# Performance work log

Hardware: AMD Instinct MI355X
Metric: run time of the kernel (lower is better)

Reference implementation:

```python
import itertools
import jax, jax.numpy as jnp
import numpy as np

N_QUBITS = 8
N_LAYERS = 2
BATCH = 8192
INPUT_DIM = 3072
NUM_CLASSES = 10

_In = np.eye(2, dtype=np.complex64)
_Xn = np.array([[0, 1], [1, 0]], dtype=np.complex64)
_Yn = np.array([[0, -1j], [1j, 0]], dtype=np.complex64)
_Zn = np.array([[1, 0], [0, -1]], dtype=np.complex64)
_P = {"I": _In, "X": _Xn, "Y": _Yn, "Z": _Zn}
_XX = jnp.asarray(np.kron(_Xn, _Xn))
_YY = jnp.asarray(np.kron(_Yn, _Yn))
_ZZ = jnp.asarray(np.kron(_Zn, _Zn))
_I4 = jnp.eye(4, dtype=jnp.complex64)
# 2-qubit Pauli words in PennyLane ArbitraryUnitary order: IX, IY, IZ, XI, ..., ZZ
_WORDS = jnp.asarray(np.stack([np.kron(_P[a], _P[b]) for a, b in itertools.product("IXYZ", repeat=2)][1:]))


def apply_gate(state, U, wires):
    """Apply a 2^k x 2^k gate U to the given wires of a (2,)*n statevector."""
    n = state.ndim
    k = len(wires)
    U = U.reshape((2,) * (2 * k)).astype(state.dtype)
    state = jnp.tensordot(U, state, axes=(list(range(k, 2 * k)), list(wires)))
    rest = [a for a in range(n) if a not in wires]
    perm = [0] * n
    for i, a in enumerate(wires):
        perm[a] = i
    for j, a in enumerate(rest):
        perm[a] = k + j
    return jnp.transpose(state, perm)


def u3_mat(t, p, d):
    ct, st = jnp.cos(t / 2).astype(jnp.complex64), jnp.sin(t / 2).astype(jnp.complex64)
    r0 = jnp.stack([ct, -jnp.exp(1j * d) * st])
    r1 = jnp.stack([jnp.exp(1j * p) * st, jnp.exp(1j * (p + d)) * ct])
    return jnp.stack([r0, r1])


def ry_mat(t):
    c, s = jnp.cos(t / 2), jnp.sin(t / 2)
    return jnp.stack([jnp.stack([c, -s]), jnp.stack([s, c])]).astype(jnp.complex64)


def ising_mat(phi, pauli2):
    # exp(-i phi/2 P) for two-qubit Pauli word P (P^2 = I)
    return jnp.cos(phi / 2) * _I4 - 1j * jnp.sin(phi / 2) * pauli2


def circuit(conv_w, pool_w, last_w, feats):
    state = jnp.zeros((2,) * N_QUBITS, jnp.complex64).at[(0,) * N_QUBITS].set(1.0)
    # AngleEmbedding with RY rotations
    for w in range(N_QUBITS):
        state = apply_gate(state, ry_mat(feats[w]), (w,))
    wires = list(range(N_QUBITS))
    for layer in range(N_LAYERS):
        cw = conv_w[layer]
        nw = len(wires)
        for p in (0, 1):
            for idx in range(nw - 1):
                if idx % 2 == p:
                    a, b = wires[idx], wires[idx + 1]
                    state = apply_gate(state, u3_mat(cw[idx, 0], cw[idx, 1], cw[idx, 2]), (a,))
                    state = apply_gate(state, u3_mat(cw[idx + 1, 3], cw[idx + 1, 4], cw[idx + 1, 5]), (b,))
                    state = apply_gate(state, ising_mat(cw[idx, 6], _ZZ), (a, b))
                    state = apply_gate(state, ising_mat(cw[idx, 7], _YY), (a, b))
                    state = apply_gate(state, ising_mat(cw[idx, 8], _XX), (a, b))
                    state = apply_gate(state, u3_mat(cw[idx, 9], cw[idx, 10], cw[idx, 11]), (a,))
                    state = apply_gate(state, u3_mat(cw[idx + 1, 12], cw[idx + 1, 13], cw[idx + 1, 14]), (b,))
        # Pooling: mid-circuit measure + conditional U3 == (deferred measurement)
        pw = pool_w[layer]
        for idx in range(1, nw, 2):
            u = u3_mat(pw[idx // 2, 0], pw[idx // 2, 1], pw[idx // 2, 2])
            cu = jnp.zeros((4, 4), jnp.complex64).at[0, 0].set(1.0).at[1, 1].set(1.0).at[2:, 2:].set(u)
            state = apply_gate(state, cu, (wires[idx], wires[idx - 1]))
        wires = wires[::2]
    # ArbitraryUnitary on remaining 2 wires: product of 15 PauliRot gates
    for k in range(15):
        mat = jnp.cos(last_w[k] / 2) * _I4 - 1j * jnp.sin(last_w[k] / 2) * _WORDS[k]
        state = apply_gate(state, mat, tuple(wires))
    probs = state.real ** 2 + state.imag ** 2
    z = jnp.sum(probs, axis=tuple(range(1, N_QUBITS)))  # (2,)
    return z[0] - z[1]


def setup_inputs() -> dict:
    key = jax.random.key(0)
    ks = jax.random.split(key, 8)
    return {
        "x": jax.random.normal(ks[0], (BATCH, INPUT_DIM), jnp.float32),
        "fc_w": jax.random.normal(ks[1], (N_QUBITS, INPUT_DIM), jnp.float32) * 0.02,
        "fc_b": jnp.zeros((N_QUBITS,), jnp.float32),
        "conv_params": jax.random.normal(ks[2], (N_LAYERS, N_QUBITS, 15), jnp.float32),
        "pool_params": jax.random.normal(ks[3], (N_LAYERS, N_QUBITS // 2, 3), jnp.float32),
        "last_params": jax.random.normal(ks[4], (15,), jnp.float32),
        "out_w": jax.random.normal(ks[5], (NUM_CLASSES, 1), jnp.float32),
        "out_b": jnp.zeros((NUM_CLASSES,), jnp.float32),
    }


def reference(x, fc_w, fc_b, conv_params, pool_params, last_params, out_w, out_b):
    feats = jnp.tanh(x.reshape(x.shape[0], -1) @ fc_w.T + fc_b)  # (B, n_qubits)
    qvals = jax.vmap(lambda f: circuit(conv_params, pool_params, last_params, f))(feats)
    logits = qvals[:, None].astype(x.dtype) @ out_w.T + out_b  # (B, num_classes)
    return logits
```

## Files before the change

kernel.cpp:

```cpp
#include <hip/hip_runtime.h>
#include <math.h>

__constant__ int G_ORD[17] = {0,1,2,3,4,5,6, 10,11,12,13, 7,8,9, 14,15, 16};
__constant__ int G_WA[17]  = {0,2,4,6,1,3,5, 1,3,5,7, 0,4,2, 2,6, 0};
__constant__ int G_WB[17]  = {1,3,5,7,2,4,6, 0,2,4,6, 2,6,4, 0,4, 4};
__constant__ int CDESC[10][3] = {{0,0,1},{0,2,3},{0,4,5},{0,6,7},{0,1,2},{0,3,4},{0,5,6},
                                 {1,0,1},{1,2,3},{1,1,2}};
__constant__ int PDESC[6][2] = {{0,0},{0,1},{0,2},{0,3},{1,0},{1,1}};
__constant__ float2 PMAT[4][4] = {
  {{1.f,0.f},{0.f,0.f},{0.f,0.f},{1.f,0.f}},
  {{0.f,0.f},{1.f,0.f},{1.f,0.f},{0.f,0.f}},
  {{0.f,0.f},{0.f,-1.f},{0.f,1.f},{0.f,0.f}},
  {{1.f,0.f},{0.f,0.f},{0.f,0.f},{-1.f,0.f}}};

__device__ __forceinline__ float2 cmul(float2 a, float2 b){
  return make_float2(a.x*b.x - a.y*b.y, a.x*b.y + a.y*b.x);
}
__device__ __forceinline__ float2 cadd(float2 a, float2 b){
  return make_float2(a.x+b.x, a.y+b.y);
}

__device__ void u3m(float t, float p, float d, float2* u){
  float ct = cosf(0.5f*t), st = sinf(0.5f*t);
  u[0] = make_float2(ct, 0.f);
  u[1] = make_float2(-cosf(d)*st, -sinf(d)*st);
  u[2] = make_float2(cosf(p)*st,  sinf(p)*st);
  u[3] = make_float2(cosf(p+d)*ct, sinf(p+d)*ct);
}

__device__ void kron2(const float2* A, const float2* B, float2* M){
  #pragma unroll
  for (int ia=0; ia<2; ia++)
    #pragma unroll
    for (int ib=0; ib<2; ib++)
      #pragma unroll
      for (int ja=0; ja<2; ja++)
        #pragma unroll
        for (int jb=0; jb<2; jb++)
          M[(ia*2+ib)*4 + (ja*2+jb)] = cmul(A[ia*2+ja], B[ib*2+jb]);
}

__device__ void mul44(const float2* A, const float2* B, float2* C){
  #pragma unroll
  for (int r=0;r<4;r++)
    #pragma unroll
    for (int c=0;c<4;c++){
      float2 s = make_float2(0.f,0.f);
      #pragma unroll
      for (int k=0;k<4;k++) s = cadd(s, cmul(A[r*4+k], B[k*4+c]));
      C[r*4+c] = s;
    }
}

__device__ void rotword(float phi, int qa, int qb, float2* R){
  float ch = cosf(0.5f*phi), sh = sinf(0.5f*phi);
  float2 W[16];
  kron2(PMAT[qa], PMAT[qb], W);
  #pragma unroll
  for (int i=0;i<16;i++) R[i] = make_float2(sh*W[i].y, -sh*W[i].x);
  #pragma unroll
  for (int d=0;d<4;d++) R[d*4+d].x += ch;
}

__global__ __launch_bounds__(64) void build_u_kernel(
    const float* __restrict__ conv, const float* __restrict__ pool,
    const float* __restrict__ last, float2* __restrict__ U){
  __shared__ float2 gl[17][16];
  __shared__ float2 st[256];
  int t = threadIdx.x, col = blockIdx.x;
  {
    float2 M[16], T[16], R[16];
    if (t < 10){
      int layer = CDESC[t][0], ra = CDESC[t][1], rb = CDESC[t][2];
      const float* cw = conv + layer*120;
      int bA = ra*15, bB = rb*15;
      float2 A1[4], B1[4], A2[4], B2[4], K[16];
      u3m(cw[bA+0], cw[bA+1], cw[bA+2], A1);
      u3m(cw[bB+3], cw[bB+4], cw[bB+5], B1);
      kron2(A1, B1, M);
      rotword(cw[bA+6], 3, 3, R); mul44(R, M, T);
      rotword(cw[bA+7], 2, 2, R); mul44(R, T, M);
      rotword(cw[bA+8], 1, 1, R); mul44(R, M, T);
      u3m(cw[bA+9],  cw[bA+10], cw[bA+11], A2);
      u3m(cw[bB+12], cw[bB+13], cw[bB+14], B2);
      kron2(A2, B2, K); mul44(K, T, M);
    } else if (t < 16){
      int layer = PDESC[t-10][0], h = PDESC[t-10][1];
      const float* pw = pool + layer*12 + h*3;
      float2 u[4];
      u3m(pw[0], pw[1], pw[2], u);
      #pragma unroll
      for (int i=0;i<16;i++) M[i] = make_float2(0.f,0.f);
      M[0]  = make_float2(1.f,0.f);
      M[5]  = make_float2(1.f,0.f);
      M[10] = u[0]; M[11] = u[1]; M[14] = u[2]; M[15] = u[3];
    } else if (t == 16){
      #pragma unroll
      for (int i=0;i<16;i++) M[i] = make_float2((i%5==0)?1.f:0.f, 0.f);
      for (int k=0;k<15;k++){
        int w = k+1;
        rotword(last[k], w>>2, w&3, R);
        mul44(R, M, T);
        #pragma unroll
        for (int i=0;i<16;i++) M[i] = T[i];
      }
    }
    if (t < 17){
      #pragma unroll
      for (int i=0;i<16;i++) gl[t][i] = M[i];
    }
  }
  #pragma unroll
  for (int k=t; k<256; k+=64) st[k] = make_float2(k==col ? 1.f : 0.f, 0.f);
  __syncthreads();
  for (int g=0; g<17; g++){
    int slot = G_ORD[g];
    float2 m[16];
    #pragma unroll
    for (int i=0;i<16;i++) m[i] = gl[slot][i];
    int pa = 7 - G_WA[g], pb = 7 - G_WB[g];
    int plo = pa < pb ? pa : pb, phi_ = pa < pb ? pb : pa;
    int mm = t;
    int t1   = ((mm >> plo) << (plo+1)) | (mm & ((1<<plo)-1));
    int base = ((t1 >> phi_) << (phi_+1)) | (t1 & ((1<<phi_)-1));
    int ba = 1<<pa, bb = 1<<pb;
    int i0 = base, i1 = base|bb, i2 = base|ba, i3 = base|ba|bb;
    float2 s0 = st[i0], s1 = st[i1], s2 = st[i2], s3 = st[i3];
    float2 n0 = cadd(cadd(cmul(m[0], s0), cmul(m[1], s1)), cadd(cmul(m[2], s2), cmul(m[3], s3)));
    float2 n1 = cadd(cadd(cmul(m[4], s0), cmul(m[5], s1)), cadd(cmul(m[6], s2), cmul(m[7], s3)));
    float2 n2 = cadd(cadd(cmul(m[8], s0), cmul(m[9], s1)), cadd(cmul(m[10],s2), cmul(m[11],s3)));
    float2 n3 = cadd(cadd(cmul(m[12],s0), cmul(m[13],s1)), cadd(cmul(m[14],s2), cmul(m[15],s3)));
    st[i0] = n0; st[i1] = n1; st[i2] = n2; st[i3] = n3;
    __syncthreads();
  }
  #pragma unroll
  for (int k=t; k<256; k+=64) U[k*256 + col] = st[k];
}

__global__ __launch_bounds__(256) void build_a_kernel(
    const float2* __restrict__ U, float* __restrict__ A){
  int j = threadIdx.x, i0 = blockIdx.x*2;
  float a0=0.f, a1=0.f;
  #pragma unroll 8
  for (int k=0; k<256; k++){
    float2 uj = U[k*256 + j];
    float2 u0 = U[k*256 + i0+0];
    float2 u1 = U[k*256 + i0+1];
    float sgn = (k < 128) ? 1.f : -1.f;
    a0 += sgn*(u0.x*uj.x + u0.y*uj.y);
    a1 += sgn*(u1.x*uj.x + u1.y*uj.y);
  }
  A[(i0+0)*256 + j] = a0;
  A[(i0+1)*256 + j] = a1;
}

__global__ __launch_bounds__(256) void main_kernel(
    const float* __restrict__ x, const float* __restrict__ fcw,
    const float* __restrict__ fcb, const float* __restrict__ Ag,
    const float* __restrict__ outw, const float* __restrict__ outb,
    float* __restrict__ out){
  __shared__ float lds[12288];
  __shared__ float flds[128];
  float* red = lds;
  float* As  = lds;
  float* ps  = lds + 8192;
  int t = threadIdx.x, lane = t & 63, wv = t >> 6, jb = lane;
  int r0 = blockIdx.x * 16;
  {
    int rw = r0 + wv*4;
    const float4* x4 = (const float4*)x;
    const float4* w4 = (const float4*)fcw;
    float acc[4][8];
    #pragma unroll
    for (int r=0;r<4;r++)
      #pragma unroll
      for (int o=0;o<8;o++) acc[r][o] = 0.f;
    #pragma unroll 2
    for (int p=0; p<12; p++){
      float4 wf[8];
      #pragma unroll
      for (int o=0;o<8;o++) wf[o] = w4[o*768 + p*64 + lane];
      #pragma unroll
      for (int r=0;r<4;r++){
        float4 xv = x4[(size_t)(rw+r)*768 + p*64 + lane];
        #pragma unroll
        for (int o=0;o<8;o++){
          acc[r][o] += xv.x*wf[o].x + xv.y*wf[o].y + xv.z*wf[o].z + xv.w*wf[o].w;
        }
      }
    }
    #pragma unroll
    for (int r=0;r<4;r++)
      #pragma unroll
      for (int o=0;o<8;o++)
        red[((wv*4+r)*8 + o)*68 + lane] = acc[r][o];
  }
  __syncthreads();
  if (t < 128){
    const float4* rp = (const float4*)(red + t*68);
    float4 s4 = make_float4(0.f,0.f,0.f,0.f);
    #pragma unroll
    for (int i=0;i<16;i++){
      float4 v = rp[i];
      s4.x += v.x; s4.y += v.y; s4.z += v.z; s4.w += v.w;
    }
    flds[t] = tanhf(s4.x + s4.y + s4.z + s4.w + fcb[t & 7]);
  }
  __syncthreads();
  float psi_local[16];
  {
    int row = t >> 4, i1 = t & 15;
    const float* f = flds + row*8;
    float c[8], s[8];
    #pragma unroll
    for (int w=0; w<8; w++){
      float a = 0.5f*f[w];
      __sincosf(a, &s[w], &c[w]);
    }
    float Hv = (i1&8 ? s[0]:c[0]) * (i1&4 ? s[1]:c[1])
             * (i1&2 ? s[2]:c[2]) * (i1&1 ? s[3]:c[3]);
    float l2[2], l4[4], l8[8], L[16];
    l2[0]=c[4]; l2[1]=s[4];
    #pragma unroll
    for (int a=0;a<2;a++){ l4[a*2]=l2[a]*c[5]; l4[a*2+1]=l2[a]*s[5]; }
    #pragma unroll
    for (int a=0;a<4;a++){ l8[a*2]=l4[a]*c[6]; l8[a*2+1]=l4[a]*s[6]; }
    #pragma unroll
    for (int a=0;a<8;a++){ L[a*2]=l8[a]*c[7]; L[a*2+1]=l8[a]*s[7]; }
    #pragma unroll
    for (int j=0;j<16;j++) psi_local[j] = Hv*L[j];
  }
  __syncthreads();
  {
    int row = t >> 4, i1 = t & 15;
    float4* dst = (float4*)(ps + row*256 + i1*16);
    #pragma unroll
    for (int qd=0; qd<4; qd++)
      dst[qd] = make_float4(psi_local[qd*4+0], psi_local[qd*4+1],
                            psi_local[qd*4+2], psi_local[qd*4+3]);
  }
  const float4* As4 = (const float4*)As;
  const float4* ps4 = (const float4*)ps;
  const float4* Ag4 = (const float4*)Ag;
  float4 acc4[4];
  #pragma unroll
  for (int r=0;r<4;r++) acc4[r] = make_float4(0.f,0.f,0.f,0.f);
  for (int chunk=0; chunk<8; chunk++){
    __syncthreads();
    #pragma unroll
    for (int pass=0; pass<8; pass++){
      int kk = pass*4 + wv;
      *(float4*)(As + kk*256 + jb*4) = Ag4[(chunk*32 + kk)*64 + jb];
    }
    __syncthreads();
    #pragma unroll
    for (int kq=0; kq<8; kq++){
      float4 av0 = As4[(kq*4+0)*64 + jb];
      float4 av1 = As4[(kq*4+1)*64 + jb];
      float4 av2 = As4[(kq*4+2)*64 + jb];
      float4 av3 = As4[(kq*4+3)*64 + jb];
      #pragma unroll
      for (int r=0; r<4; r++){
        float4 pv = ps4[(wv*4+r)*64 + chunk*8 + kq];
        acc4[r].x += pv.x*av0.x + pv.y*av1.x + pv.z*av2.x + pv.w*av3.x;
        acc4[r].y += pv.x*av0.y + pv.y*av1.y + pv.z*av2.y + pv.w*av3.y;
        acc4[r].z += pv.x*av0.z + pv.y*av1.z + pv.z*av2.z + pv.w*av3.z;
        acc4[r].w += pv.x*av0.w + pv.y*av1.w + pv.z*av2.w + pv.w*av3.w;
      }
    }
  }
  float p[4];
  #pragma unroll
  for (int r=0; r<4; r++){
    float4 psv = ps4[(wv*4+r)*64 + jb];
    float pr = acc4[r].x*psv.x + acc4[r].y*psv.y + acc4[r].z*psv.z + acc4[r].w*psv.w;
    #pragma unroll
    for (int m=1; m<64; m<<=1) pr += __shfl_xor(pr, m, 64);
    p[r] = pr;
  }
  if (jb < 40){
    int ridx = jb / 10, c = jb - ridx*10;
    float q = (ridx==0) ? p[0] : (ridx==1) ? p[1] : (ridx==2) ? p[2] : p[3];
    out[(r0 + wv*4 + ridx)*10 + c] = q*outw[c] + outb[c];
  }
}

extern "C" void kernel_launch(void* const* d_in, const int* in_sizes, int n_in,
                              void* d_out, int out_size, void* d_ws, size_t ws_size,
                              hipStream_t stream) {
  const float* x    = (const float*)d_in[0];
  const float* fcw  = (const float*)d_in[1];
  const float* fcb  = (const float*)d_in[2];
  const float* conv = (const float*)d_in[3];
  const float* pool = (const float*)d_in[4];
  const float* last = (const float*)d_in[5];
  const float* outw = (const float*)d_in[6];
  const float* outb = (const float*)d_in[7];
  float* out = (float*)d_out;

  float* ws = (float*)d_ws;
  float2* U  = (float2*)ws;
  float*  Am = ws + 131072;

  build_u_kernel<<<256, 64, 0, stream>>>(conv, pool, last, U);
  build_a_kernel<<<128, 256, 0, stream>>>(U, Am);
  main_kernel<<<512, 256, 0, stream>>>(x, fcw, fcb, Am, outw, outb, out);
}
```

Measured before the change: 244.7 us.

## Split quadratic-form K dimension across eight waves and read A directly from global

Blocks grow from 256 to 512 threads. The quadratic form psi^T A psi is now split along the K dimension: each of the eight waves covers 32 rows of A for all 16 batch rows and reads A straight from global (L2) instead of staging chunks in LDS behind repeated barriers. Per-wave partial results are reduced through a small shared array. LDS use drops, which allows more resident blocks, but each thread now holds 16 float4 accumulators, raising register pressure, and the fc stage gives each wave only 2 rows.

```diff
diff --git a/kernel.cpp b/kernel.cpp
--- a/kernel.cpp
+++ b/kernel.cpp
@@ -154,25 +154,25 @@
   A[(i0+1)*256 + j] = a1;
 }
 
-__global__ __launch_bounds__(256) void main_kernel(
+__global__ __launch_bounds__(512, 4) void main_kernel(
     const float* __restrict__ x, const float* __restrict__ fcw,
     const float* __restrict__ fcb, const float* __restrict__ Ag,
     const float* __restrict__ outw, const float* __restrict__ outb,
     float* __restrict__ out){
-  __shared__ float lds[12288];
+  __shared__ float lds[8704];
   __shared__ float flds[128];
+  __shared__ float qpart[8][16];
   float* red = lds;
-  float* As  = lds;
-  float* ps  = lds + 8192;
+  float* ps  = lds;
   int t = threadIdx.x, lane = t & 63, wv = t >> 6, jb = lane;
   int r0 = blockIdx.x * 16;
   {
-    int rw = r0 + wv*4;
+    int rw = r0 + wv*2;
     const float4* x4 = (const float4*)x;
     const float4* w4 = (const float4*)fcw;
-    float acc[4][8];
-    #pragma unroll
-    for (int r=0;r<4;r++)
+    float acc[2][8];
+    #pragma unroll
+    for (int r=0;r<2;r++)
       #pragma unroll
       for (int o=0;o<8;o++) acc[r][o] = 0.f;
     #pragma unroll 2
@@ -181,7 +181,7 @@
       #pragma unroll
       for (int o=0;o<8;o++) wf[o] = w4[o*768 + p*64 + lane];
       #pragma unroll
-      for (int r=0;r<4;r++){
+      for (int r=0;r<2;r++){
         float4 xv = x4[(size_t)(rw+r)*768 + p*64 + lane];
         #pragma unroll
         for (int o=0;o<8;o++){
@@ -190,10 +190,10 @@
       }
     }
     #pragma unroll
-    for (int r=0;r<4;r++)
+    for (int r=0;r<2;r++)
       #pragma unroll
       for (int o=0;o<8;o++)
-        red[((wv*4+r)*8 + o)*68 + lane] = acc[r][o];
+        red[((wv*2+r)*8 + o)*68 + lane] = acc[r][o];
   }
   __syncthreads();
   if (t < 128){
@@ -207,8 +207,7 @@
     flds[t] = tanhf(s4.x + s4.y + s4.z + s4.w + fcb[t & 7]);
   }
   __syncthreads();
-  float psi_local[16];
-  {
+  if (t < 256){
     int row = t >> 4, i1 = t & 15;
     const float* f = flds + row*8;
     float c[8], s[8];
@@ -227,61 +226,48 @@
     for (int a=0;a<4;a++){ l8[a*2]=l4[a]*c[6]; l8[a*2+1]=l4[a]*s[6]; }
     #pragma unroll
     for (int a=0;a<8;a++){ L[a*2]=l8[a]*c[7]; L[a*2+1]=l8[a]*s[7]; }
-    #pragma unroll
-    for (int j=0;j<16;j++) psi_local[j] = Hv*L[j];
-  }
-  __syncthreads();
-  {
-    int row = t >> 4, i1 = t & 15;
     float4* dst = (float4*)(ps + row*256 + i1*16);
     #pragma unroll
     for (int qd=0; qd<4; qd++)
-      dst[qd] = make_float4(psi_local[qd*4+0], psi_local[qd*4+1],
-                            psi_local[qd*4+2], psi_local[qd*4+3]);
-  }
-  const float4* As4 = (const float4*)As;
+      dst[qd] = make_float4(Hv*L[qd*4+0], Hv*L[qd*4+1], Hv*L[qd*4+2], Hv*L[qd*4+3]);
+  }
+  __syncthreads();
   const float4* ps4 = (const float4*)ps;
   const float4* Ag4 = (const float4*)Ag;
-  float4 acc4[4];
-  #pragma unroll
-  for (int r=0;r<4;r++) acc4[r] = make_float4(0.f,0.f,0.f,0.f);
-  for (int chunk=0; chunk<8; chunk++){
-    __syncthreads();
-    #pragma unroll
-    for (int pass=0; pass<8; pass++){
-      int kk = pass*4 + wv;
-      *(float4*)(As + kk*256 + jb*4) = Ag4[(chunk*32 + kk)*64 + jb];
-    }
-    __syncthreads();
-    #pragma unroll
-    for (int kq=0; kq<8; kq++){
-      float4 av0 = As4[(kq*4+0)*64 + jb];
-      float4 av1 = As4[(kq*4+1)*64 + jb];
-      float4 av2 = As4[(kq*4+2)*64 + jb];
-      float4 av3 = As4[(kq*4+3)*64 + jb];
-      #pragma unroll
-      for (int r=0; r<4; r++){
-        float4 pv = ps4[(wv*4+r)*64 + chunk*8 + kq];
-        acc4[r].x += pv.x*av0.x + pv.y*av1.x + pv.z*av2.x + pv.w*av3.x;
-        acc4[r].y += pv.x*av0.y + pv.y*av1.y + pv.z*av2.y + pv.w*av3.y;
-        acc4[r].z += pv.x*av0.z + pv.y*av1.z + pv.z*av2.z + pv.w*av3.z;
-        acc4[r].w += pv.x*av0.w + pv.y*av1.w + pv.z*av2.w + pv.w*av3.w;
-      }
-    }
-  }
-  float p[4];
-  #pragma unroll
-  for (int r=0; r<4; r++){
-    float4 psv = ps4[(wv*4+r)*64 + jb];
-    float pr = acc4[r].x*psv.x + acc4[r].y*psv.y + acc4[r].z*psv.z + acc4[r].w*psv.w;
-    #pragma unroll
-    for (int m=1; m<64; m<<=1) pr += __shfl_xor(pr, m, 64);
-    p[r] = pr;
-  }
-  if (jb < 40){
-    int ridx = jb / 10, c = jb - ridx*10;
-    float q = (ridx==0) ? p[0] : (ridx==1) ? p[1] : (ridx==2) ? p[2] : p[3];
-    out[(r0 + wv*4 + ridx)*10 + c] = q*outw[c] + outb[c];
+  float4 acc4[16];
+  #pragma unroll
+  for (int r=0;r<16;r++) acc4[r] = make_float4(0.f,0.f,0.f,0.f);
+  #pragma unroll 2
+  for (int g=0; g<8; g++){
+    int k = wv*32 + g*4;
+    float4 a0 = Ag4[(k+0)*64 + jb];
+    float4 a1 = Ag4[(k+1)*64 + jb];
+    float4 a2 = Ag4[(k+2)*64 + jb];
+    float4 a3 = Ag4[(k+3)*64 + jb];
+    #pragma unroll
+    for (int r=0; r<16; r++){
+      float4 pk = ps4[r*64 + wv*8 + g];
+      acc4[r].x += pk.x*a0.x + pk.y*a1.x + pk.z*a2.x + pk.w*a3.x;
+      acc4[r].y += pk.x*a0.y + pk.y*a1.y + pk.z*a2.y + pk.w*a3.y;
+      acc4[r].z += pk.x*a0.z + pk.y*a1.z + pk.z*a2.z + pk.w*a3.z;
+      acc4[r].w += pk.x*a0.w + pk.y*a1.w + pk.z*a2.w + pk.w*a3.w;
+    }
+  }
+  #pragma unroll
+  for (int r=0; r<16; r++){
+    float4 pc = ps4[r*64 + jb];
+    float q = acc4[r].x*pc.x + acc4[r].y*pc.y + acc4[r].z*pc.z + acc4[r].w*pc.w;
+    #pragma unroll
+    for (int m=1; m<64; m<<=1) q += __shfl_xor(q, m, 64);
+    if (lane == 0) qpart[wv][r] = q;
+  }
+  __syncthreads();
+  if (t < 160){
+    int row = t / 10, c = t - row*10;
+    float q = 0.f;
+    #pragma unroll
+    for (int w=0; w<8; w++) q += qpart[w][row];
+    out[(r0 + row)*10 + c] = q*outw[c] + outb[c];
   }
 }
 
@@ -304,5 +290,5 @@
 
   build_u_kernel<<<256, 64, 0, stream>>>(conv, pool, last, U);
   build_a_kernel<<<128, 256, 0, stream>>>(U, Am);
-  main_kernel<<<512, 256, 0, stream>>>(x, fcw, fcb, Am, outw, outb, out);
-}
+  main_kernel<<<512, 512, 0, stream>>>(x, fcw, fcb, Am, outw, outb, out);
+}
```

Result: slower. 365.5 us (+49.4%).
